# Optimization experiments

Measured on AMD Instinct MI355X. Metric: run time of the kernel, lower is better.

## Reference

```python
import jax, jax.numpy as jnp
import numpy as np

G, N, E = 8, 10000, 160000
D_IN, D_H, D_OUT = 300, 256, 128
EPS = 1e-5


def setup_inputs() -> dict:
    key = jax.random.key(0)
    ks = jax.random.split(key, 4)
    x = jax.random.normal(ks[0], (G, N, D_IN), dtype=jnp.float32)
    edge_index = jax.random.randint(ks[1], (G, 2, E), 0, N)
    W1 = jax.random.normal(ks[2], (D_IN, D_H), dtype=jnp.float32) * (1.0 / np.sqrt(D_IN))
    b1 = jnp.zeros((D_H,), jnp.float32)
    g1 = jnp.ones((D_H,), jnp.float32)
    be1 = jnp.zeros((D_H,), jnp.float32)
    W2 = jax.random.normal(ks[3], (D_H, D_OUT), dtype=jnp.float32) * (1.0 / np.sqrt(D_H))
    b2 = jnp.zeros((D_OUT,), jnp.float32)
    g2 = jnp.ones((D_OUT,), jnp.float32)
    be2 = jnp.zeros((D_OUT,), jnp.float32)
    return dict(x=x, edge_index=edge_index, W1=W1, b1=b1, g1=g1, be1=be1,
                W2=W2, b2=b2, g2=g2, be2=be2)


def _gcn_conv(x, src, dst, W, b):
    # PyG GCNConv: h = xW; add self-loops; sym-normalized aggregation; + bias
    h = x @ W                                   # [N, F_out]
    deg = jnp.ones((N,), h.dtype).at[dst].add(1.0)  # in-degree + self-loop
    dinv = jax.lax.rsqrt(deg)                   # deg >= 1 always
    coef = dinv[src] * dinv[dst]                # [E]
    agg = jax.ops.segment_sum(h[src] * coef[:, None], dst, num_segments=N)
    agg = agg + h * (dinv * dinv)[:, None]      # self-loop term
    return agg + b


def _layernorm(x, g, b):
    mu = jnp.mean(x, axis=-1, keepdims=True)
    var = jnp.mean(jnp.square(x - mu), axis=-1, keepdims=True)
    return (x - mu) * jax.lax.rsqrt(var + EPS) * g + b


def _forward_one(xg, eg, W1, b1, g1, be1, W2, b2, g2, be2):
    src, dst = eg[0], eg[1]
    h = jax.nn.relu(_gcn_conv(xg, src, dst, W1, b1))
    h = _layernorm(h, g1, be1)
    h = _gcn_conv(h, src, dst, W2, b2)
    return _layernorm(h, g2, be2)


def reference(x, edge_index, W1, b1, g1, be1, W2, b2, g2, be2):
    f = jax.vmap(lambda xg, eg: _forward_one(xg, eg, W1, b1, g1, be1, W2, b2, g2, be2))
    return f(x, edge_index)  # [G, N, D_OUT]
```

## Files before the change

### kernel.cpp

```cpp
#include <hip/hip_runtime.h>
#include <hip/hip_bf16.h>

#define GG   8
#define NN   10000
#define EE   160000
#define DIN  300
#define KP1  320
#define DH   256
#define DOUT 128
#define LN_EPS 1e-5f

typedef short bf16x8 __attribute__((ext_vector_type(8)));
typedef float f32x4  __attribute__((ext_vector_type(4)));
typedef ushort u16x8 __attribute__((ext_vector_type(8)));

__device__ inline float bf2f(ushort u) {
    union { unsigned int i; float f; } x;
    x.i = ((unsigned int)u) << 16;
    return x.f;
}
__device__ inline ushort f2b(float f) {
    union { float f; unsigned int u; } x;
    x.f = f;
    unsigned int u = x.u;
    return (ushort)((u + 0x7fffu + ((u >> 16) & 1u)) >> 16);
}
__device__ inline short bcvt(float f) {
    __hip_bfloat16 h = __float2bfloat16(f);
    return *reinterpret_cast<short*>(&h);
}

__global__ __launch_bounds__(256) void k_util(const float* __restrict__ W1,
                                              const float* __restrict__ W2,
                                              ushort* __restrict__ w1t,
                                              ushort* __restrict__ w2t,
                                              int* __restrict__ cnt) {
    int i = blockIdx.x * blockDim.x + threadIdx.x;
    if (i < GG * NN) cnt[i] = 0;
    if (i < DH * KP1) {
        int n = i / KP1, k = i % KP1;
        w1t[i] = (k < DIN) ? f2b(W1[(size_t)k * DH + n]) : 0;
    }
    if (i < DOUT * DH) {
        int n = i / DH, k = i % DH;
        w2t[i] = f2b(W2[(size_t)k * DOUT + n]);
    }
}

__global__ __launch_bounds__(256) void k_count(const int* __restrict__ ei,
                                               int* __restrict__ cnt,
                                               int* __restrict__ slot) {
    int bid = blockIdx.x;
    int g = bid & 7;
    int e = (bid >> 3) * 256 + threadIdx.x;
    int dst = ei[(size_t)g * 2 * EE + EE + e];
    slot[(size_t)g * EE + e] = atomicAdd(&cnt[g * NN + dst], 1);
}

__global__ void k_scan(const int* __restrict__ cnt, int* __restrict__ rowptr,
                       float* __restrict__ dinv) {
    int g = blockIdx.x;
    int t = threadIdx.x;
    const int per = (NN + 255) / 256;
    __shared__ int sums[256];
    __shared__ int offs[257];
    int base = t * per;
    int s = 0;
    for (int i = 0; i < per; i++) {
        int n = base + i;
        if (n < NN) s += cnt[g * NN + n];
    }
    sums[t] = s;
    __syncthreads();
    if (t == 0) {
        int acc = 0;
        for (int i = 0; i < 256; i++) { offs[i] = acc; acc += sums[i]; }
        offs[256] = acc;
    }
    __syncthreads();
    int run = offs[t];
    for (int i = 0; i < per; i++) {
        int n = base + i;
        if (n < NN) {
            int c = cnt[g * NN + n];
            rowptr[g * (NN + 1) + n] = run;
            dinv[g * NN + n] = 1.0f / sqrtf(1.0f + (float)c);
            run += c;
        }
    }
    if (t == 255) rowptr[g * (NN + 1) + NN] = offs[256];
}

__global__ __launch_bounds__(256) void k_fill(const int* __restrict__ ei,
                                              const int* __restrict__ rowptr,
                                              const int* __restrict__ slot,
                                              const float* __restrict__ dinv,
                                              int2* __restrict__ edges) {
    int bid = blockIdx.x;
    int g = bid & 7;
    int e = (bid >> 3) * 256 + threadIdx.x;
    int src = ei[(size_t)g * 2 * EE + e];
    int dst = ei[(size_t)g * 2 * EE + EE + e];
    int pos = rowptr[g * (NN + 1) + dst] + slot[(size_t)g * EE + e];
    float coef = dinv[g * NN + src] * dinv[g * NN + dst];
    int2 rec;
    rec.x = src;
    rec.y = __float_as_int(coef);
    edges[(size_t)g * EE + pos] = rec;
}

__global__ __launch_bounds__(512) void k_gemm1(const float* __restrict__ x,
                                               const ushort* __restrict__ Bt,
                                               ushort* __restrict__ C) {
    __shared__ float  As[128 * 36];
    __shared__ ushort Bs[256 * 32];
    const int tid = threadIdx.x;
    const int lane = tid & 63;
    const int w = tid >> 6;
    const int wm = w >> 2;
    const int wn = w & 3;
    const int m0 = blockIdx.x * 128;

    const int fr = lane & 15;
    const int fk = (lane >> 4) * 8;

    const int arow = tid >> 2;
    const int acol = (tid & 3) * 8;
    const float* xr = x + (size_t)(m0 + arow) * DIN;

    const int brow = tid >> 2;
    const int bcol = (tid & 3) * 8;

    f32x4 acc[4][4];
#pragma unroll
    for (int i = 0; i < 4; i++)
#pragma unroll
        for (int j = 0; j < 4; j++) acc[i][j] = (f32x4){0.f, 0.f, 0.f, 0.f};

    float4 a0 = *(const float4*)(xr + min(acol, DIN - 4));
    float4 a1 = *(const float4*)(xr + min(acol + 4, DIN - 4));

    for (int k0 = 0; k0 < KP1; k0 += 32) {
        *(float4*)&As[arow * 36 + acol] = a0;
        *(float4*)&As[arow * 36 + acol + 4] = a1;
#pragma unroll
        for (int r = 0; r < 2; r++) {
            const ushort* gb = &Bt[(size_t)(r * 128 + brow) * KP1 + k0 + bcol];
            __builtin_amdgcn_global_load_lds(
                (const __attribute__((address_space(1))) void*)gb,
                (__attribute__((address_space(3))) void*)&Bs[(r * 128 + (tid >> 6) * 16) * 32],
                16, 0, 0);
        }
        {
            const int kn = k0 + 32;
            a0 = *(const float4*)(xr + min(kn + acol, DIN - 4));
            a1 = *(const float4*)(xr + min(kn + acol + 4, DIN - 4));
        }
        __syncthreads();
        bf16x8 af[4], bfv[4];
#pragma unroll
        for (int i = 0; i < 4; i++) {
            const float* ap = &As[(wm * 64 + i * 16 + fr) * 36 + fk];
            f32x4 p = *(const f32x4*)ap;
            f32x4 q = *(const f32x4*)(ap + 4);
            af[i][0] = bcvt(p[0]); af[i][1] = bcvt(p[1]);
            af[i][2] = bcvt(p[2]); af[i][3] = bcvt(p[3]);
            af[i][4] = bcvt(q[0]); af[i][5] = bcvt(q[1]);
            af[i][6] = bcvt(q[2]); af[i][7] = bcvt(q[3]);
            bfv[i] = *(const bf16x8*)&Bs[(wn * 64 + i * 16 + fr) * 32 + fk];
        }
#pragma unroll
        for (int i = 0; i < 4; i++)
#pragma unroll
            for (int j = 0; j < 4; j++)
                acc[i][j] = __builtin_amdgcn_mfma_f32_16x16x32_bf16(af[i], bfv[j],
                                                                    acc[i][j], 0, 0, 0);
        __syncthreads();
    }

#pragma unroll
    for (int i = 0; i < 4; i++) {
        int row0 = m0 + wm * 64 + i * 16 + (lane >> 4) * 4;
#pragma unroll
        for (int j = 0; j < 4; j++) {
            int col = wn * 64 + j * 16 + fr;
#pragma unroll
            for (int q = 0; q < 4; q++) {
                C[(size_t)(row0 + q) * DH + col] = f2b(acc[i][j][q]);
            }
        }
    }
}

template <int KPAD>
__global__ __launch_bounds__(256) void k_gemm_mfma(const ushort* __restrict__ A,
                                                   const ushort* __restrict__ Bt,
                                                   ushort* __restrict__ C, int Ntot) {
    __shared__ ushort As[128 * 32];
    __shared__ ushort Bs[128 * 32];
    const int tid = threadIdx.x;
    const int lane = tid & 63;
    const int w = tid >> 6;
    const int wm = w >> 1, wn = w & 1;
    const int m0 = blockIdx.x * 128;
    const int n0 = blockIdx.y * 128;

    const int srow = tid >> 2;
    const int scole = (tid & 3) * 8;

    const int fr = lane & 15;
    const int fk = (lane >> 4) * 8;

    f32x4 acc[4][4];
#pragma unroll
    for (int i = 0; i < 4; i++)
#pragma unroll
        for (int j = 0; j < 4; j++) acc[i][j] = (f32x4){0.f, 0.f, 0.f, 0.f};

    for (int k0 = 0; k0 < KPAD; k0 += 32) {
#pragma unroll
        for (int r = 0; r < 2; r++) {
            const ushort* ga = &A[(size_t)(m0 + r * 64 + srow) * KPAD + k0 + scole];
            __builtin_amdgcn_global_load_lds(
                (const __attribute__((address_space(1))) void*)ga,
                (__attribute__((address_space(3))) void*)&As[(r * 64 + w * 16) * 32],
                16, 0, 0);
            const ushort* gb = &Bt[(size_t)(n0 + r * 64 + srow) * KPAD + k0 + scole];
            __builtin_amdgcn_global_load_lds(
                (const __attribute__((address_space(1))) void*)gb,
                (__attribute__((address_space(3))) void*)&Bs[(r * 64 + w * 16) * 32],
                16, 0, 0);
        }
        __syncthreads();
        bf16x8 af[4], bfv[4];
#pragma unroll
        for (int i = 0; i < 4; i++) {
            af[i]  = *(const bf16x8*)&As[(wm * 64 + i * 16 + fr) * 32 + fk];
            bfv[i] = *(const bf16x8*)&Bs[(wn * 64 + i * 16 + fr) * 32 + fk];
        }
#pragma unroll
        for (int i = 0; i < 4; i++)
#pragma unroll
            for (int j = 0; j < 4; j++)
                acc[i][j] = __builtin_amdgcn_mfma_f32_16x16x32_bf16(af[i], bfv[j],
                                                                    acc[i][j], 0, 0, 0);
        __syncthreads();
    }

#pragma unroll
    for (int i = 0; i < 4; i++) {
        int row0 = m0 + wm * 64 + i * 16 + (lane >> 4) * 4;
#pragma unroll
        for (int j = 0; j < 4; j++) {
            int col = n0 + wn * 64 + j * 16 + fr;
#pragma unroll
            for (int q = 0; q < 4; q++) {
                C[(size_t)(row0 + q) * Ntot + col] = f2b(acc[i][j][q]);
            }
        }
    }
}

template <int D, bool RELU, typename OutT>
__global__ __launch_bounds__(256) void k_agg(const ushort* __restrict__ h,
                                             const int* __restrict__ rowptr,
                                             const int2* __restrict__ edges,
                                             const float* __restrict__ dinv,
                                             const float* __restrict__ bias,
                                             const float* __restrict__ gam,
                                             const float* __restrict__ bet,
                                             OutT* __restrict__ out) {
    constexpr int F = 8;
    constexpr int GL = D / F;
    constexpr int NPW = 64 / GL;
    __shared__ int2 s_rec[4][64];
    const int tid = threadIdx.x;
    const int lane = tid & 63;
    const int wv = tid >> 6;
    const int grp = lane / GL;
    const int gl = lane & (GL - 1);
    const int fb = gl * F;
    const int g = blockIdx.x & 7;
    const int n = (blockIdx.x >> 3) * (4 * NPW) + wv * NPW + grp;
    const ushort* hg = h + (size_t)g * NN * D;
    const int2* eg = edges + (size_t)g * EE;
    const int r0 = rowptr[g * (NN + 1) + n];
    const int r1 = rowptr[g * (NN + 1) + n + 1];
    const float dn = dinv[g * NN + n];
    int2* srw = &s_rec[wv][grp * GL];

    float acc[F];
#pragma unroll
    for (int i = 0; i < F; i++) acc[i] = 0.f;

    for (int base = r0; base < r1; base += GL) {
        const int c = min(GL, r1 - base);
        int2 rec;
        rec.x = 0;
        rec.y = 0;
        if (gl < c) rec = eg[base + gl];
        srw[gl] = rec;
        const int cpad = (c + 3) & ~3;
        for (int j = 0; j < cpad; j += 4) {
            const int4 ra = *(const int4*)&srw[j];
            const int4 rb = *(const int4*)&srw[j + 2];
            u16x8 v0 = *(const u16x8*)&hg[(size_t)ra.x * D + fb];
            u16x8 v1 = *(const u16x8*)&hg[(size_t)ra.z * D + fb];
            u16x8 v2 = *(const u16x8*)&hg[(size_t)rb.x * D + fb];
            u16x8 v3 = *(const u16x8*)&hg[(size_t)rb.z * D + fb];
            const float w0 = __int_as_float(ra.y);
            const float w1 = __int_as_float(ra.w);
            const float w2 = __int_as_float(rb.y);
            const float w3 = __int_as_float(rb.w);
#pragma unroll
            for (int i = 0; i < F; i++) acc[i] = fmaf(bf2f(v0[i]), w0, acc[i]);
#pragma unroll
            for (int i = 0; i < F; i++) acc[i] = fmaf(bf2f(v1[i]), w1, acc[i]);
#pragma unroll
            for (int i = 0; i < F; i++) acc[i] = fmaf(bf2f(v2[i]), w2, acc[i]);
#pragma unroll
            for (int i = 0; i < F; i++) acc[i] = fmaf(bf2f(v3[i]), w3, acc[i]);
        }
    }

    {
        const float ws = dn * dn;
        u16x8 v = *(const u16x8*)&hg[(size_t)n * D + fb];
#pragma unroll
        for (int i = 0; i < F; i++) {
            acc[i] = fmaf(bf2f(v[i]), ws, acc[i]);
            acc[i] += bias[fb + i];
            if (RELU) acc[i] = fmaxf(acc[i], 0.f);
        }
    }
    float s1 = 0.f, s2 = 0.f;
#pragma unroll
    for (int i = 0; i < F; i++) { s1 += acc[i]; s2 += acc[i] * acc[i]; }
#pragma unroll
    for (int o = GL / 2; o > 0; o >>= 1) {
        s1 += __shfl_xor(s1, o);
        s2 += __shfl_xor(s2, o);
    }
    const float mu = s1 / D;
    const float rs = rsqrtf(s2 / D - mu * mu + LN_EPS);

    if constexpr (sizeof(OutT) == 2) {
        u16x8 o;
#pragma unroll
        for (int i = 0; i < F; i++)
            o[i] = f2b((acc[i] - mu) * rs * gam[fb + i] + bet[fb + i]);
        *(u16x8*)&((ushort*)out)[((size_t)g * NN + n) * D + fb] = o;
    } else {
        float* op = &((float*)out)[((size_t)g * NN + n) * D + fb];
        float4 oa, ob;
        oa.x = (acc[0] - mu) * rs * gam[fb + 0] + bet[fb + 0];
        oa.y = (acc[1] - mu) * rs * gam[fb + 1] + bet[fb + 1];
        oa.z = (acc[2] - mu) * rs * gam[fb + 2] + bet[fb + 2];
        oa.w = (acc[3] - mu) * rs * gam[fb + 3] + bet[fb + 3];
        ob.x = (acc[4] - mu) * rs * gam[fb + 4] + bet[fb + 4];
        ob.y = (acc[5] - mu) * rs * gam[fb + 5] + bet[fb + 5];
        ob.z = (acc[6] - mu) * rs * gam[fb + 6] + bet[fb + 6];
        ob.w = (acc[7] - mu) * rs * gam[fb + 7] + bet[fb + 7];
        *(float4*)&op[0] = oa;
        *(float4*)&op[4] = ob;
    }
}

extern "C" void kernel_launch(void* const* d_in, const int* in_sizes, int n_in,
                              void* d_out, int out_size, void* d_ws, size_t ws_size,
                              hipStream_t stream) {
    const float* x   = (const float*)d_in[0];
    const int*   ei  = (const int*)d_in[1];
    const float* W1  = (const float*)d_in[2];
    const float* b1  = (const float*)d_in[3];
    const float* g1  = (const float*)d_in[4];
    const float* be1 = (const float*)d_in[5];
    const float* W2  = (const float*)d_in[6];
    const float* b2  = (const float*)d_in[7];
    const float* g2  = (const float*)d_in[8];
    const float* be2 = (const float*)d_in[9];
    float* out = (float*)d_out;

    char* w = (char*)d_ws;
    ushort* w1t  = (ushort*)w;                        w += (size_t)DH * KP1 * 2;
    ushort* w2t  = (ushort*)w;                        w += (size_t)DOUT * DH * 2;
    ushort* h1b  = (ushort*)w;                        w += (size_t)80000 * DH * 2;
    ushort* out1 = (ushort*)w;                        w += (size_t)80000 * DH * 2;
    int*   cnt    = (int*)w;                          w += (size_t)GG * NN * 4;
    int*   rowptr = (int*)w;                          w += (size_t)GG * (NN + 1) * 4 + 224;
    int*   slot   = (int*)w;                          w += (size_t)GG * EE * 4;
    float* dinv   = (float*)w;                        w += (size_t)GG * NN * 4;
    int2*  edges  = (int2*)w;
    ushort* h2b = h1b;

    k_util<<<dim3((DH * KP1 + 255) / 256), dim3(256), 0, stream>>>(W1, W2, w1t, w2t, cnt);

    k_count<<<dim3((EE / 256) * GG), dim3(256), 0, stream>>>(ei, cnt, slot);
    k_scan<<<dim3(GG), dim3(256), 0, stream>>>(cnt, rowptr, dinv);
    k_fill<<<dim3((EE / 256) * GG), dim3(256), 0, stream>>>(ei, rowptr, slot, dinv, edges);

    k_gemm1<<<dim3(80000 / 128), dim3(512), 0, stream>>>(x, w1t, h1b);

    k_agg<DH, true, ushort><<<dim3((NN / 8) * GG), dim3(256), 0, stream>>>(
        h1b, rowptr, edges, dinv, b1, g1, be1, out1);

    k_gemm_mfma<DH><<<dim3(80000 / 128, DOUT / 128), dim3(256), 0, stream>>>(out1, w2t, h2b, DOUT);

    k_agg<DOUT, false, float><<<dim3((NN / 16) * GG), dim3(256), 0, stream>>>(
        h2b, rowptr, edges, dinv, b2, g2, be2, out);
}
```

Before: 227.1 us.

## Restructure GEMMs to keep full weight slice resident in LDS, stream A from global

Both GEMM kernels now load the whole needed weight slice (64-column slab of W1, or all of W2) into padded shared memory once per block. Each wave then reads its A rows straight from global memory into MFMA fragments, with no per-k-step barriers or A staging in LDS. GEMM1 is split across 4 column blocks, so x rows are re-read up to 4 times, presumably served from cache. The aim is to remove per-iteration __syncthreads and LDS round-trips for A, in exchange for uncoalesced fragment-shaped global loads of A.

```diff
diff --git a/kernel.cpp b/kernel.cpp
--- a/kernel.cpp
+++ b/kernel.cpp
@@ -8,6 +8,7 @@
 #define KP1  320
 #define DH   256
 #define DOUT 128
+#define MTOT 80000
 #define LN_EPS 1e-5f
 
 typedef short bf16x8 __attribute__((ext_vector_type(8)));
@@ -112,150 +113,121 @@
 __global__ __launch_bounds__(512) void k_gemm1(const float* __restrict__ x,
                                                const ushort* __restrict__ Bt,
                                                ushort* __restrict__ C) {
-    __shared__ float  As[128 * 36];
-    __shared__ ushort Bs[256 * 32];
+    __shared__ ushort Bs[64 * 328];
     const int tid = threadIdx.x;
     const int lane = tid & 63;
     const int w = tid >> 6;
-    const int wm = w >> 2;
-    const int wn = w & 3;
-    const int m0 = blockIdx.x * 128;
-
+    const int n0 = blockIdx.x * 64;
     const int fr = lane & 15;
     const int fk = (lane >> 4) * 8;
 
-    const int arow = tid >> 2;
-    const int acol = (tid & 3) * 8;
-    const float* xr = x + (size_t)(m0 + arow) * DIN;
-
-    const int brow = tid >> 2;
-    const int bcol = (tid & 3) * 8;
-
-    f32x4 acc[4][4];
-#pragma unroll
-    for (int i = 0; i < 4; i++)
-#pragma unroll
-        for (int j = 0; j < 4; j++) acc[i][j] = (f32x4){0.f, 0.f, 0.f, 0.f};
-
-    float4 a0 = *(const float4*)(xr + min(acol, DIN - 4));
-    float4 a1 = *(const float4*)(xr + min(acol + 4, DIN - 4));
-
-    for (int k0 = 0; k0 < KP1; k0 += 32) {
-        *(float4*)&As[arow * 36 + acol] = a0;
-        *(float4*)&As[arow * 36 + acol + 4] = a1;
-#pragma unroll
-        for (int r = 0; r < 2; r++) {
-            const ushort* gb = &Bt[(size_t)(r * 128 + brow) * KP1 + k0 + bcol];
-            __builtin_amdgcn_global_load_lds(
-                (const __attribute__((address_space(1))) void*)gb,
-                (__attribute__((address_space(3))) void*)&Bs[(r * 128 + (tid >> 6) * 16) * 32],
-                16, 0, 0);
-        }
-        {
-            const int kn = k0 + 32;
-            a0 = *(const float4*)(xr + min(kn + acol, DIN - 4));
-            a1 = *(const float4*)(xr + min(kn + acol + 4, DIN - 4));
-        }
-        __syncthreads();
-        bf16x8 af[4], bfv[4];
-#pragma unroll
-        for (int i = 0; i < 4; i++) {
-            const float* ap = &As[(wm * 64 + i * 16 + fr) * 36 + fk];
-            f32x4 p = *(const f32x4*)ap;
-            f32x4 q = *(const f32x4*)(ap + 4);
-            af[i][0] = bcvt(p[0]); af[i][1] = bcvt(p[1]);
-            af[i][2] = bcvt(p[2]); af[i][3] = bcvt(p[3]);
-            af[i][4] = bcvt(q[0]); af[i][5] = bcvt(q[1]);
-            af[i][6] = bcvt(q[2]); af[i][7] = bcvt(q[3]);
-            bfv[i] = *(const bf16x8*)&Bs[(wn * 64 + i * 16 + fr) * 32 + fk];
-        }
-#pragma unroll
-        for (int i = 0; i < 4; i++)
-#pragma unroll
-            for (int j = 0; j < 4; j++)
-                acc[i][j] = __builtin_amdgcn_mfma_f32_16x16x32_bf16(af[i], bfv[j],
-                                                                    acc[i][j], 0, 0, 0);
-        __syncthreads();
-    }
-
-#pragma unroll
-    for (int i = 0; i < 4; i++) {
-        int row0 = m0 + wm * 64 + i * 16 + (lane >> 4) * 4;
+    for (int idx = tid; idx < 64 * 40; idx += 512) {
+        const int r = idx / 40, c8 = (idx - r * 40) * 8;
+        *(u16x8*)&Bs[r * 328 + c8] = *(const u16x8*)&Bt[(size_t)(n0 + r) * KP1 + c8];
+    }
+    __syncthreads();
+
+    const int rbase = blockIdx.y * 256 + w * 32;
+    const float* xr0 = x + (size_t)min(rbase + fr,      MTOT - 1) * DIN;
+    const float* xr1 = x + (size_t)min(rbase + 16 + fr, MTOT - 1) * DIN;
+
+    f32x4 acc[2][4];
+#pragma unroll
+    for (int g = 0; g < 2; g++)
+#pragma unroll
+        for (int j = 0; j < 4; j++) acc[g][j] = (f32x4){0.f, 0.f, 0.f, 0.f};
+
+#pragma unroll
+    for (int kk = 0; kk < 10; kk++) {
+        const int kb = kk * 32 + fk;
+        const int c0 = min(kb, DIN - 4);
+        const int c1 = min(kb + 4, DIN - 4);
+        f32x4 p0 = *(const f32x4*)(xr0 + c0);
+        f32x4 q0 = *(const f32x4*)(xr0 + c1);
+        f32x4 p1 = *(const f32x4*)(xr1 + c0);
+        f32x4 q1 = *(const f32x4*)(xr1 + c1);
+        bf16x8 a0, a1;
+        a0[0] = bcvt(p0[0]); a0[1] = bcvt(p0[1]); a0[2] = bcvt(p0[2]); a0[3] = bcvt(p0[3]);
+        a0[4] = bcvt(q0[0]); a0[5] = bcvt(q0[1]); a0[6] = bcvt(q0[2]); a0[7] = bcvt(q0[3]);
+        a1[0] = bcvt(p1[0]); a1[1] = bcvt(p1[1]); a1[2] = bcvt(p1[2]); a1[3] = bcvt(p1[3]);
+        a1[4] = bcvt(q1[0]); a1[5] = bcvt(q1[1]); a1[6] = bcvt(q1[2]); a1[7] = bcvt(q1[3]);
+        bf16x8 bv[4];
+#pragma unroll
+        for (int j = 0; j < 4; j++)
+            bv[j] = *(const bf16x8*)&Bs[(j * 16 + fr) * 328 + kb];
 #pragma unroll
         for (int j = 0; j < 4; j++) {
-            int col = wn * 64 + j * 16 + fr;
+            acc[0][j] = __builtin_amdgcn_mfma_f32_16x16x32_bf16(a0, bv[j], acc[0][j], 0, 0, 0);
+            acc[1][j] = __builtin_amdgcn_mfma_f32_16x16x32_bf16(a1, bv[j], acc[1][j], 0, 0, 0);
+        }
+    }
+
+#pragma unroll
+    for (int g = 0; g < 2; g++) {
+        const int row0 = rbase + g * 16 + (lane >> 4) * 4;
+#pragma unroll
+        for (int j = 0; j < 4; j++) {
+            const int col = n0 + j * 16 + fr;
 #pragma unroll
             for (int q = 0; q < 4; q++) {
-                C[(size_t)(row0 + q) * DH + col] = f2b(acc[i][j][q]);
+                const int row = row0 + q;
+                if (row < MTOT)
+                    C[(size_t)row * DH + col] = f2b(acc[g][j][q]);
             }
         }
     }
 }
 
-template <int KPAD>
-__global__ __launch_bounds__(256) void k_gemm_mfma(const ushort* __restrict__ A,
-                                                   const ushort* __restrict__ Bt,
-                                                   ushort* __restrict__ C, int Ntot) {
-    __shared__ ushort As[128 * 32];
-    __shared__ ushort Bs[128 * 32];
+__global__ __launch_bounds__(512) void k_gemm2(const ushort* __restrict__ A,
+                                               const ushort* __restrict__ Bt,
+                                               ushort* __restrict__ C) {
+    __shared__ ushort Bs[128 * 264];
     const int tid = threadIdx.x;
     const int lane = tid & 63;
     const int w = tid >> 6;
-    const int wm = w >> 1, wn = w & 1;
-    const int m0 = blockIdx.x * 128;
-    const int n0 = blockIdx.y * 128;
-
-    const int srow = tid >> 2;
-    const int scole = (tid & 3) * 8;
-
     const int fr = lane & 15;
     const int fk = (lane >> 4) * 8;
 
-    f32x4 acc[4][4];
-#pragma unroll
-    for (int i = 0; i < 4; i++)
-#pragma unroll
-        for (int j = 0; j < 4; j++) acc[i][j] = (f32x4){0.f, 0.f, 0.f, 0.f};
-
-    for (int k0 = 0; k0 < KPAD; k0 += 32) {
-#pragma unroll
-        for (int r = 0; r < 2; r++) {
-            const ushort* ga = &A[(size_t)(m0 + r * 64 + srow) * KPAD + k0 + scole];
-            __builtin_amdgcn_global_load_lds(
-                (const __attribute__((address_space(1))) void*)ga,
-                (__attribute__((address_space(3))) void*)&As[(r * 64 + w * 16) * 32],
-                16, 0, 0);
-            const ushort* gb = &Bt[(size_t)(n0 + r * 64 + srow) * KPAD + k0 + scole];
-            __builtin_amdgcn_global_load_lds(
-                (const __attribute__((address_space(1))) void*)gb,
-                (__attribute__((address_space(3))) void*)&Bs[(r * 64 + w * 16) * 32],
-                16, 0, 0);
-        }
-        __syncthreads();
-        bf16x8 af[4], bfv[4];
-#pragma unroll
-        for (int i = 0; i < 4; i++) {
-            af[i]  = *(const bf16x8*)&As[(wm * 64 + i * 16 + fr) * 32 + fk];
-            bfv[i] = *(const bf16x8*)&Bs[(wn * 64 + i * 16 + fr) * 32 + fk];
-        }
-#pragma unroll
-        for (int i = 0; i < 4; i++)
-#pragma unroll
-            for (int j = 0; j < 4; j++)
-                acc[i][j] = __builtin_amdgcn_mfma_f32_16x16x32_bf16(af[i], bfv[j],
-                                                                    acc[i][j], 0, 0, 0);
-        __syncthreads();
-    }
-
-#pragma unroll
-    for (int i = 0; i < 4; i++) {
-        int row0 = m0 + wm * 64 + i * 16 + (lane >> 4) * 4;
-#pragma unroll
-        for (int j = 0; j < 4; j++) {
-            int col = n0 + wn * 64 + j * 16 + fr;
+    for (int idx = tid; idx < 128 * 32; idx += 512) {
+        const int r = idx >> 5, c8 = (idx & 31) * 8;
+        *(u16x8*)&Bs[r * 264 + c8] = *(const u16x8*)&Bt[(size_t)r * DH + c8];
+    }
+    __syncthreads();
+
+    const int rbase = blockIdx.x * 256 + w * 32;
+    const ushort* ar0 = A + (size_t)min(rbase + fr,      MTOT - 1) * DH;
+    const ushort* ar1 = A + (size_t)min(rbase + 16 + fr, MTOT - 1) * DH;
+
+    f32x4 acc[2][8];
+#pragma unroll
+    for (int g = 0; g < 2; g++)
+#pragma unroll
+        for (int j = 0; j < 8; j++) acc[g][j] = (f32x4){0.f, 0.f, 0.f, 0.f};
+
+#pragma unroll
+    for (int kk = 0; kk < 8; kk++) {
+        const int kb = kk * 32 + fk;
+        bf16x8 a0 = *(const bf16x8*)(ar0 + kb);
+        bf16x8 a1 = *(const bf16x8*)(ar1 + kb);
+#pragma unroll
+        for (int j = 0; j < 8; j++) {
+            bf16x8 bv = *(const bf16x8*)&Bs[(j * 16 + fr) * 264 + kb];
+            acc[0][j] = __builtin_amdgcn_mfma_f32_16x16x32_bf16(a0, bv, acc[0][j], 0, 0, 0);
+            acc[1][j] = __builtin_amdgcn_mfma_f32_16x16x32_bf16(a1, bv, acc[1][j], 0, 0, 0);
+        }
+    }
+
+#pragma unroll
+    for (int g = 0; g < 2; g++) {
+        const int row0 = rbase + g * 16 + (lane >> 4) * 4;
+#pragma unroll
+        for (int j = 0; j < 8; j++) {
+            const int col = j * 16 + fr;
 #pragma unroll
             for (int q = 0; q < 4; q++) {
-                C[(size_t)(row0 + q) * Ntot + col] = f2b(acc[i][j][q]);
+                const int row = row0 + q;
+                if (row < MTOT)
+                    C[(size_t)row * DOUT + col] = f2b(acc[g][j][q]);
             }
         }
     }
@@ -384,8 +356,8 @@
     char* w = (char*)d_ws;
     ushort* w1t  = (ushort*)w;                        w += (size_t)DH * KP1 * 2;
     ushort* w2t  = (ushort*)w;                        w += (size_t)DOUT * DH * 2;
-    ushort* h1b  = (ushort*)w;                        w += (size_t)80000 * DH * 2;
-    ushort* out1 = (ushort*)w;                        w += (size_t)80000 * DH * 2;
+    ushort* h1b  = (ushort*)w;                        w += (size_t)MTOT * DH * 2;
+    ushort* out1 = (ushort*)w;                        w += (size_t)MTOT * DH * 2;
     int*   cnt    = (int*)w;                          w += (size_t)GG * NN * 4;
     int*   rowptr = (int*)w;                          w += (size_t)GG * (NN + 1) * 4 + 224;
     int*   slot   = (int*)w;                          w += (size_t)GG * EE * 4;
@@ -399,12 +371,12 @@
     k_scan<<<dim3(GG), dim3(256), 0, stream>>>(cnt, rowptr, dinv);
     k_fill<<<dim3((EE / 256) * GG), dim3(256), 0, stream>>>(ei, rowptr, slot, dinv, edges);
 
-    k_gemm1<<<dim3(80000 / 128), dim3(512), 0, stream>>>(x, w1t, h1b);
+    k_gemm1<<<dim3(4, (MTOT + 255) / 256), dim3(512), 0, stream>>>(x, w1t, h1b);
 
     k_agg<DH, true, ushort><<<dim3((NN / 8) * GG), dim3(256), 0, stream>>>(
         h1b, rowptr, edges, dinv, b1, g1, be1, out1);
 
-    k_gemm_mfma<DH><<<dim3(80000 / 128, DOUT / 128), dim3(256), 0, stream>>>(out1, w2t, h2b, DOUT);
+    k_gemm2<<<dim3((MTOT + 255) / 256), dim3(512), 0, stream>>>(out1, w2t, h2b);
 
     k_agg<DOUT, false, float><<<dim3((NN / 16) * GG), dim3(256), 0, stream>>>(
         h2b, rowptr, edges, dinv, b2, g2, be2, out);
```

New measurement: 267.0 us. 1.18x slower.
